# Kernel optimization log

Hardware: AMD Instinct MI355X
Metric: run time of the kernel (lower is better)

Reference implementation:

```python
import jax, jax.numpy as jnp
import numpy as np

N_NODES = 50000
N_EDGES = 800000
IN_DIM = 128
OUT_DIM = 128


def setup_inputs() -> dict:
    key = jax.random.key(0)
    k1, k2, k3, k4, k5 = jax.random.split(key, 5)
    x = jax.random.normal(k1, (N_NODES, IN_DIM), dtype=jnp.float32)
    # Xavier-uniform-ish scale for the two weight matrices
    scale = float(np.sqrt(6.0 / (IN_DIM + OUT_DIM)))
    Wg = jax.random.uniform(k2, (OUT_DIM, IN_DIM), dtype=jnp.float32, minval=-scale, maxval=scale)
    Wl = jax.random.uniform(k3, (OUT_DIM, IN_DIM), dtype=jnp.float32, minval=-scale, maxval=scale)
    bias = jnp.zeros((OUT_DIM,), dtype=jnp.float32)
    neigh_idx = jax.random.randint(k4, (N_EDGES,), 0, N_NODES, dtype=jnp.int32)
    seg_ids = jnp.sort(jax.random.randint(k5, (N_EDGES,), 0, N_NODES, dtype=jnp.int32))
    return {"x": x, "Wg": Wg, "Wl": Wl, "bias": bias,
            "neigh_idx": neigh_idx, "seg_ids": seg_ids}


def reference(x, Wg, Wl, bias, neigh_idx, seg_ids):
    N = x.shape[0]
    # global 1x1 map on all nodes (self path)
    global_maps = x @ Wg.T                                  # [N, out]
    # per-edge neighbor features: local + global maps of the neighbor
    neigh_x = x[neigh_idx]                                  # [E, in]
    mixed = neigh_x @ Wl.T + global_maps[neigh_idx]         # [E, out]
    # segment-mean over each destination node's neighbors
    sums = jax.ops.segment_sum(mixed, seg_ids, num_segments=N)            # [N, out]
    cnt = jax.ops.segment_sum(jnp.ones((seg_ids.shape[0],), x.dtype), seg_ids, num_segments=N)  # [N]
    mean = sums / jnp.maximum(cnt, 1.0)[:, None]
    # deg == 0 nodes: neigh_agg falls back to global_maps (as in the torch loop)
    neigh_agg = jnp.where((cnt > 0)[:, None], mean, global_maps)
    out = neigh_agg + global_maps + bias
    return jax.nn.elu(out)
```

## Files before the change

kernel.cpp:

```cpp
#include <hip/hip_runtime.h>
#include <hip/hip_bf16.h>

#define NN 50000
#define NE 800000
#define DIM 128

typedef float f32x4 __attribute__((ext_vector_type(4)));
typedef __bf16 bf16x8 __attribute__((ext_vector_type(8)));

__global__ void build_v(const float* __restrict__ Wg, const float* __restrict__ Wl,
                        __bf16* __restrict__ V) {
    int i = blockIdx.x * blockDim.x + threadIdx.x;
    if (i >= DIM * 256) return;
    int d = i >> 8;
    int k = i & 255;
    float v;
    if (k < DIM) v = Wg[d * DIM + k];
    else         v = Wg[d * DIM + (k - DIM)] + Wl[d * DIM + (k - DIM)];
    V[i] = (__bf16)v;
}

__global__ void build_off(const int* __restrict__ seg, int* __restrict__ off) {
    int n = blockIdx.x * blockDim.x + threadIdx.x;
    if (n > NN) return;
    int lo = 0, hi = NE;
    while (lo < hi) {
        int mid = (lo + hi) >> 1;
        if (seg[mid] < n) lo = mid + 1; else hi = mid;
    }
    off[n] = lo;
}

__global__ void __launch_bounds__(128) seg_mean(const float* __restrict__ x,
        const int* __restrict__ nidx, const int* __restrict__ off,
        int* __restrict__ cnt_ws, __bf16* __restrict__ meanb) {
    int n = blockIdx.x;
    int t = threadIdx.x;
    int s = off[n], e = off[n + 1];
    float sum = 0.f;
    int i = s;
    for (; i + 2 <= e; i += 2) {
        int i0 = nidx[i], i1 = nidx[i + 1];
        float a = x[i0 * DIM + t];
        float b = x[i1 * DIM + t];
        sum += a + b;
    }
    if (i < e) sum += x[nidx[i] * DIM + t];
    int c = e - s;
    float mean = c > 0 ? sum / (float)c : 0.f;
    meanb[n * DIM + t] = (__bf16)mean;
    if (t == 0) cnt_ws[n] = c;
}

__global__ void __launch_bounds__(64) gemm_ep(const float* __restrict__ x,
        const __bf16* __restrict__ meanb, const __bf16* __restrict__ V,
        const float* __restrict__ bias, const int* __restrict__ cnt_ws,
        float* __restrict__ out) {
    int m0 = blockIdx.x * 16;
    int lane = threadIdx.x;
    int rowin = lane & 15;
    int kg = lane >> 4;
    int row = m0 + rowin;

    f32x4 acc[8] = {};

    #pragma unroll
    for (int s = 0; s < 4; ++s) {
        int k0 = s * 32 + kg * 8;
        const float* xp = x + row * DIM + k0;
        f32x4 v0 = *reinterpret_cast<const f32x4*>(xp);
        f32x4 v1 = *reinterpret_cast<const f32x4*>(xp + 4);
        bf16x8 a;
        a[0]=(__bf16)v0[0]; a[1]=(__bf16)v0[1]; a[2]=(__bf16)v0[2]; a[3]=(__bf16)v0[3];
        a[4]=(__bf16)v1[0]; a[5]=(__bf16)v1[1]; a[6]=(__bf16)v1[2]; a[7]=(__bf16)v1[3];
        #pragma unroll
        for (int f = 0; f < 8; ++f) {
            int d = f * 16 + rowin;
            bf16x8 b = *reinterpret_cast<const bf16x8*>(&V[d * 256 + k0]);
            acc[f] = __builtin_amdgcn_mfma_f32_16x16x32_bf16(a, b, acc[f], 0, 0, 0);
        }
    }
    #pragma unroll
    for (int s = 0; s < 4; ++s) {
        int k0 = s * 32 + kg * 8;
        bf16x8 a = *reinterpret_cast<const bf16x8*>(&meanb[row * DIM + k0]);
        #pragma unroll
        for (int f = 0; f < 8; ++f) {
            int d = f * 16 + rowin;
            bf16x8 b = *reinterpret_cast<const bf16x8*>(&V[d * 256 + 128 + k0]);
            acc[f] = __builtin_amdgcn_mfma_f32_16x16x32_bf16(a, b, acc[f], 0, 0, 0);
        }
    }

    int colin = lane & 15;
    int rbase = (lane >> 4) * 4;
    int cz[4];
    #pragma unroll
    for (int r = 0; r < 4; ++r) cz[r] = cnt_ws[m0 + rbase + r];
    #pragma unroll
    for (int f = 0; f < 8; ++f) {
        int d = f * 16 + colin;
        float bs = bias[d];
        #pragma unroll
        for (int r = 0; r < 4; ++r) {
            int n = m0 + rbase + r;
            float v = acc[f][r];
            float z = v + (cz[r] == 0 ? v : 0.f) + bs;
            out[n * DIM + d] = z > 0.f ? z : expm1f(z);
        }
    }
}

extern "C" void kernel_launch(void* const* d_in, const int* in_sizes, int n_in,
                              void* d_out, int out_size, void* d_ws, size_t ws_size,
                              hipStream_t stream) {
    const float* x    = (const float*)d_in[0];
    const float* Wg   = (const float*)d_in[1];
    const float* Wl   = (const float*)d_in[2];
    const float* bias = (const float*)d_in[3];
    const int*   nidx = (const int*)d_in[4];
    const int*   seg  = (const int*)d_in[5];
    float* out = (float*)d_out;

    char* p = (char*)d_ws;
    __bf16* V = (__bf16*)p;       p += DIM * 256 * 2;
    int* off = (int*)p;           p += (((NN + 1) * 4) + 511) & ~511ull;
    int* cnt = (int*)p;           p += ((NN * 4) + 511) & ~511ull;
    __bf16* meanb = (__bf16*)p;

    build_v  <<<(DIM * 256 + 255) / 256, 256, 0, stream>>>(Wg, Wl, V);
    build_off<<<(NN + 1 + 255) / 256,   256, 0, stream>>>(seg, off);
    seg_mean <<<NN, 128, 0, stream>>>(x, nidx, off, cnt, meanb);
    gemm_ep  <<<NN / 16, 64, 0, stream>>>(x, meanb, V, bias, cnt, out);
}
```

Baseline: 182.3 us.

## Pre-convert x to bf16 for the gather and cache weight fragments in persistent GEMM

Adds a pass that converts x to bf16 once, so the segment-mean gather reads half the bytes per neighbour row. The gather now runs one wavefront per node, with packed bf16 pairs and a 4-way unrolled loop. The GEMM becomes a persistent kernel in which each wave keeps its slice of the weight matrix in registers across tiles, rather than reloading V for every 16-row tile. The trade-offs are an extra kernel launch, a bf16 copy of x in workspace, and more register pressure from the held fragments.

Result: faster. 155.7 us (-14.6%).

```diff
diff --git a/kernel.cpp b/kernel.cpp
--- a/kernel.cpp
+++ b/kernel.cpp
@@ -4,9 +4,21 @@
 #define NN 50000
 #define NE 800000
 #define DIM 128
+#define NTILES (NN / 16)
+#define GEMM_BLOCKS 784
 
 typedef float f32x4 __attribute__((ext_vector_type(4)));
 typedef __bf16 bf16x8 __attribute__((ext_vector_type(8)));
+
+static __device__ __forceinline__ float bflo(unsigned v) {
+    unsigned b = v << 16; return __builtin_bit_cast(float, b);
+}
+static __device__ __forceinline__ float bfhi(unsigned v) {
+    unsigned b = v & 0xffff0000u; return __builtin_bit_cast(float, b);
+}
+static __device__ __forceinline__ unsigned short bfbits(float f) {
+    __bf16 b = (__bf16)f; return __builtin_bit_cast(unsigned short, b);
+}
 
 __global__ void build_v(const float* __restrict__ Wg, const float* __restrict__ Wl,
                         __bf16* __restrict__ V) {
@@ -20,6 +32,17 @@
     V[i] = (__bf16)v;
 }
 
+__global__ void xb_conv(const float* __restrict__ x, __bf16* __restrict__ xb) {
+    int i = blockIdx.x * blockDim.x + threadIdx.x;
+    const float* p = x + i * 8;
+    f32x4 v0 = *reinterpret_cast<const f32x4*>(p);
+    f32x4 v1 = *reinterpret_cast<const f32x4*>(p + 4);
+    bf16x8 o;
+    o[0]=(__bf16)v0[0]; o[1]=(__bf16)v0[1]; o[2]=(__bf16)v0[2]; o[3]=(__bf16)v0[3];
+    o[4]=(__bf16)v1[0]; o[5]=(__bf16)v1[1]; o[6]=(__bf16)v1[2]; o[7]=(__bf16)v1[3];
+    *reinterpret_cast<bf16x8*>(xb + i * 8) = o;
+}
+
 __global__ void build_off(const int* __restrict__ seg, int* __restrict__ off) {
     int n = blockIdx.x * blockDim.x + threadIdx.x;
     if (n > NN) return;
@@ -31,82 +54,85 @@
     off[n] = lo;
 }
 
-__global__ void __launch_bounds__(128) seg_mean(const float* __restrict__ x,
+__global__ void __launch_bounds__(256) seg_mean(const __bf16* __restrict__ xb,
         const int* __restrict__ nidx, const int* __restrict__ off,
         int* __restrict__ cnt_ws, __bf16* __restrict__ meanb) {
-    int n = blockIdx.x;
-    int t = threadIdx.x;
+    int n = blockIdx.x * 4 + (threadIdx.x >> 6);
+    if (n >= NN) return;
+    int lane = threadIdx.x & 63;
     int s = off[n], e = off[n + 1];
-    float sum = 0.f;
+    const unsigned* xu = reinterpret_cast<const unsigned*>(xb);
+    float s0 = 0.f, s1 = 0.f;
     int i = s;
-    for (; i + 2 <= e; i += 2) {
-        int i0 = nidx[i], i1 = nidx[i + 1];
-        float a = x[i0 * DIM + t];
-        float b = x[i1 * DIM + t];
-        sum += a + b;
+    for (; i + 4 <= e; i += 4) {
+        int i0 = nidx[i], i1 = nidx[i+1], i2 = nidx[i+2], i3 = nidx[i+3];
+        unsigned v0 = xu[i0 * 64 + lane];
+        unsigned v1 = xu[i1 * 64 + lane];
+        unsigned v2 = xu[i2 * 64 + lane];
+        unsigned v3 = xu[i3 * 64 + lane];
+        s0 += bflo(v0) + bflo(v1) + bflo(v2) + bflo(v3);
+        s1 += bfhi(v0) + bfhi(v1) + bfhi(v2) + bfhi(v3);
     }
-    if (i < e) sum += x[nidx[i] * DIM + t];
+    for (; i < e; ++i) {
+        unsigned v = xu[nidx[i] * 64 + lane];
+        s0 += bflo(v);
+        s1 += bfhi(v);
+    }
     int c = e - s;
-    float mean = c > 0 ? sum / (float)c : 0.f;
-    meanb[n * DIM + t] = (__bf16)mean;
-    if (t == 0) cnt_ws[n] = c;
+    float inv = c > 0 ? 1.f / (float)c : 0.f;
+    unsigned o = (unsigned)bfbits(s0 * inv) | ((unsigned)bfbits(s1 * inv) << 16);
+    reinterpret_cast<unsigned*>(meanb)[n * 64 + lane] = o;
+    if (lane == 0) cnt_ws[n] = c;
 }
 
-__global__ void __launch_bounds__(64) gemm_ep(const float* __restrict__ x,
+__global__ void __launch_bounds__(256) gemm_ep(const __bf16* __restrict__ xb,
         const __bf16* __restrict__ meanb, const __bf16* __restrict__ V,
         const float* __restrict__ bias, const int* __restrict__ cnt_ws,
         float* __restrict__ out) {
-    int m0 = blockIdx.x * 16;
-    int lane = threadIdx.x;
+    int tid = threadIdx.x;
+    int w = tid >> 6;
+    int lane = tid & 63;
     int rowin = lane & 15;
     int kg = lane >> 4;
-    int row = m0 + rowin;
+    int rbase = kg * 4;
 
-    f32x4 acc[8] = {};
+    bf16x8 Bf[8][2];
+    #pragma unroll
+    for (int s = 0; s < 8; ++s)
+        #pragma unroll
+        for (int ff = 0; ff < 2; ++ff) {
+            int d = (w * 2 + ff) * 16 + rowin;
+            Bf[s][ff] = *reinterpret_cast<const bf16x8*>(&V[d * 256 + s * 32 + kg * 8]);
+        }
+    float bs0 = bias[(w * 2) * 16 + rowin];
+    float bs1 = bias[(w * 2 + 1) * 16 + rowin];
 
-    #pragma unroll
-    for (int s = 0; s < 4; ++s) {
-        int k0 = s * 32 + kg * 8;
-        const float* xp = x + row * DIM + k0;
-        f32x4 v0 = *reinterpret_cast<const f32x4*>(xp);
-        f32x4 v1 = *reinterpret_cast<const f32x4*>(xp + 4);
-        bf16x8 a;
-        a[0]=(__bf16)v0[0]; a[1]=(__bf16)v0[1]; a[2]=(__bf16)v0[2]; a[3]=(__bf16)v0[3];
-        a[4]=(__bf16)v1[0]; a[5]=(__bf16)v1[1]; a[6]=(__bf16)v1[2]; a[7]=(__bf16)v1[3];
+    for (int t = blockIdx.x; t < NTILES; t += gridDim.x) {
+        int m0 = t * 16;
+        int row = m0 + rowin;
+        f32x4 acc0 = {}, acc1 = {};
         #pragma unroll
-        for (int f = 0; f < 8; ++f) {
-            int d = f * 16 + rowin;
-            bf16x8 b = *reinterpret_cast<const bf16x8*>(&V[d * 256 + k0]);
-            acc[f] = __builtin_amdgcn_mfma_f32_16x16x32_bf16(a, b, acc[f], 0, 0, 0);
+        for (int s = 0; s < 4; ++s) {
+            bf16x8 a = *reinterpret_cast<const bf16x8*>(&xb[row * DIM + s * 32 + kg * 8]);
+            acc0 = __builtin_amdgcn_mfma_f32_16x16x32_bf16(a, Bf[s][0], acc0, 0, 0, 0);
+            acc1 = __builtin_amdgcn_mfma_f32_16x16x32_bf16(a, Bf[s][1], acc1, 0, 0, 0);
         }
-    }
-    #pragma unroll
-    for (int s = 0; s < 4; ++s) {
-        int k0 = s * 32 + kg * 8;
-        bf16x8 a = *reinterpret_cast<const bf16x8*>(&meanb[row * DIM + k0]);
         #pragma unroll
-        for (int f = 0; f < 8; ++f) {
-            int d = f * 16 + rowin;
-            bf16x8 b = *reinterpret_cast<const bf16x8*>(&V[d * 256 + 128 + k0]);
-            acc[f] = __builtin_amdgcn_mfma_f32_16x16x32_bf16(a, b, acc[f], 0, 0, 0);
+        for (int s = 0; s < 4; ++s) {
+            bf16x8 a = *reinterpret_cast<const bf16x8*>(&meanb[row * DIM + s * 32 + kg * 8]);
+            acc0 = __builtin_amdgcn_mfma_f32_16x16x32_bf16(a, Bf[s + 4][0], acc0, 0, 0, 0);
+            acc1 = __builtin_amdgcn_mfma_f32_16x16x32_bf16(a, Bf[s + 4][1], acc1, 0, 0, 0);
         }
-    }
-
-    int colin = lane & 15;
-    int rbase = (lane >> 4) * 4;
-    int cz[4];
-    #pragma unroll
-    for (int r = 0; r < 4; ++r) cz[r] = cnt_ws[m0 + rbase + r];
-    #pragma unroll
-    for (int f = 0; f < 8; ++f) {
-        int d = f * 16 + colin;
-        float bs = bias[d];
         #pragma unroll
         for (int r = 0; r < 4; ++r) {
             int n = m0 + rbase + r;
-            float v = acc[f][r];
-            float z = v + (cz[r] == 0 ? v : 0.f) + bs;
-            out[n * DIM + d] = z > 0.f ? z : expm1f(z);
+            int c = cnt_ws[n];
+            float v0 = acc0[r];
+            float z0 = v0 + (c == 0 ? v0 : 0.f) + bs0;
+            out[n * DIM + (w * 2) * 16 + rowin] = z0 > 0.f ? z0 : expm1f(z0);
+            float v1 = acc1[r];
+            float z1 = v1 + (c == 0 ? v1 : 0.f) + bs1;
+            out[n * DIM + (w * 2 + 1) * 16 + rowin] = z1 > 0.f ? z1 : expm1f(z1);
         }
     }
 }
@@ -126,10 +152,12 @@
     __bf16* V = (__bf16*)p;       p += DIM * 256 * 2;
     int* off = (int*)p;           p += (((NN + 1) * 4) + 511) & ~511ull;
     int* cnt = (int*)p;           p += ((NN * 4) + 511) & ~511ull;
-    __bf16* meanb = (__bf16*)p;
+    __bf16* meanb = (__bf16*)p;   p += (size_t)NN * DIM * 2;
+    __bf16* xb = (__bf16*)p;
 
     build_v  <<<(DIM * 256 + 255) / 256, 256, 0, stream>>>(Wg, Wl, V);
-    build_off<<<(NN + 1 + 255) / 256,   256, 0, stream>>>(seg, off);
-    seg_mean <<<NN, 128, 0, stream>>>(x, nidx, off, cnt, meanb);
-    gemm_ep  <<<NN / 16, 64, 0, stream>>>(x, meanb, V, bias, cnt, out);
+    xb_conv  <<<(NN * DIM / 8) / 256, 256, 0, stream>>>(x, xb);
+    build_off<<<(NN + 1 + 255) / 256, 256, 0, stream>>>(seg, off);
+    seg_mean <<<(NN + 3) / 4, 256, 0, stream>>>(xb, nidx, off, cnt, meanb);
+    gemm_ep  <<<GEMM_BLOCKS, 256, 0, stream>>>(xb, meanb, V, bias, cnt, out);
 }
```
